# Optimization experiments

Measured on AMD Instinct MI355X. Metric: run time of the kernel, lower is better.

## Reference

```python
import jax, jax.numpy as jnp
import numpy as np

# Transformer config constants (from init_kwargs)
SRF = 3.0                 # spatial_receptive_field
SRF2 = SRF * SRF
ALPHA = 2.0
BETA = 8.0
GAMMA = 16.0
RES = jnp.array([0.5, 0.5, 0.5], dtype=jnp.float32)   # relative_positional_gresolution
N_BUCKETS = 2 * 8 + 1                                  # 2*beta + 1 = 17
MUL = jnp.array([N_BUCKETS ** 2, N_BUCKETS, 1], dtype=jnp.float32)  # [289,17,1]
SLICES_PER_ROT = 2


def setup_inputs() -> dict:
    key = jax.random.key(0)
    k1, k2 = jax.random.split(key)
    N = 3072
    # LiDAR-like point coordinates in a 10m cube; receptive field 3.0 makes radius filter selective
    xyz = jax.random.uniform(k1, (N, 3), dtype=jnp.float32) * 10.0
    # grid columns: [batch, block, gx, gy, gz]; values < 128 per the torch assert
    grid = jax.random.randint(k2, (N, 5), 0, 8, dtype=jnp.int32)
    return {"xyz": xyz, "grid": grid}


def _bucket_base(x):
    # from_dxyz_to_bucket_base, res.size(0)==3 branch
    x = x / RES
    x_abs = jnp.abs(x)
    log_ratio = jnp.log(jnp.maximum(x_abs, 1e-6) / ALPHA) / np.log(GAMMA / ALPHA)
    sup = jnp.minimum(jnp.round(ALPHA - (BETA - ALPHA) * log_ratio), BETA)
    sup = jnp.sign(x) * sup
    return BETA + jnp.where(x_abs <= ALPHA, jnp.round(x), sup)


def reference(xyz, grid):
    # no-kvp path of jit_compute_interactions, expressed as dense [N,N] pair masks
    batch = grid[:, 0]
    block = grid[:, 1]
    coords = grid[:, 2:]            # grid_look[:, 1:]

    # batch equality filter (meshgrid + batch==batch)
    batch_eq = batch[:, None] == batch[None, :]
    # causal block filter: block[iq] <= block[ik]
    block_le = block[:, None] <= block[None, :]

    # force_keep_neighbours: adjacent voxels within the same block
    coord_adj = jnp.max(jnp.abs(coords[:, None, :] - coords[None, :, :]), axis=-1) <= 1
    forcekeep = coord_adj & (block[:, None] == block[None, :])

    # coarse spatial hash on xy: ceil(xy / srf), neighbor cells only
    xy_coarse = jnp.ceil(xyz[:, :2] / SRF).astype(jnp.int32)
    keep_coarse = jnp.max(jnp.abs(xy_coarse[:, None, :] - xy_coarse[None, :, :]), axis=-1) <= 1

    # pairwise deltas (torch uses fp16 here; fp32 kept for numerical clarity) [N,N,3]
    dxyz = xyz[:, None, :] - xyz[None, :, :]
    keepr = jnp.sum(dxyz * dxyz, axis=-1) <= SRF2

    mask = batch_eq & block_le & (forcekeep | keep_coarse) & (forcekeep | keepr)

    dxyz_m = jnp.where(mask[..., None], dxyz, 0.0)

    # from_dxyz_to_bucket_mul: log-bucketize each axis, flatten via mul_buckets
    buckets = jnp.sum(MUL * _bucket_base(dxyz_m), axis=-1).astype(jnp.int32)
    buckets = jnp.where(mask, buckets, 0)

    # dscanid = scanid[ik] - scanid[iq], scanid = block // slices_per_rotation
    scanid = block // SLICES_PER_ROT
    dscanid = jnp.where(mask, scanid[None, :] - scanid[:, None], 0)

    return dxyz_m, buckets, dscanid, mask
```

## Files before the change

kernel.cpp:

```cpp
#include <hip/hip_runtime.h>
#include <cmath>


__device__ __forceinline__ float bucket_base(float v) {
    const float x  = v * 2.0f;
    const float xa = fabsf(x);
    if (xa <= 2.0f) {
        return 8.0f + rintf(x);
    }
    const float lr = logf(fmaxf(xa, 1e-6f) * 0.5f) / 2.0794415416798357f;
    const float sup = fminf(rintf(2.0f - 6.0f * lr), 8.0f);
    return 8.0f + ((x > 0.0f) ? sup : -sup);
}

__global__ __launch_bounds__(256) void pair_kernel(
    const float* __restrict__ xyz, const int* __restrict__ grid,
    float* __restrict__ out, int N) {
#pragma clang fp contract(off)
    const int jq = blockIdx.x * blockDim.x + threadIdx.x;
    const int j0 = jq << 2;
    const int i  = blockIdx.y;
    if (j0 >= N) return;

    const float xi = xyz[3 * i + 0];
    const float yi = xyz[3 * i + 1];
    const float zi = xyz[3 * i + 2];
    const int bat_i = grid[5 * i + 0];
    const int blk_i = grid[5 * i + 1];
    const int c0i = grid[5 * i + 2];
    const int c1i = grid[5 * i + 3];
    const int c2i = grid[5 * i + 4];
    const int xci = (int)ceilf(xi / 3.0f);
    const int yci = (int)ceilf(yi / 3.0f);
    const int scan_i = blk_i >> 1;

    const float4* pv = reinterpret_cast<const float4*>(xyz + (size_t)3 * j0);
    const float4 p0 = pv[0], p1 = pv[1], p2 = pv[2];
    const int4* gv = reinterpret_cast<const int4*>(grid + (size_t)5 * j0);
    const int4 g0 = gv[0], g1 = gv[1], g2 = gv[2], g3 = gv[3], g4 = gv[4];

    const float jx[4]  = {p0.x, p0.w, p1.z, p2.y};
    const float jy[4]  = {p0.y, p1.x, p1.w, p2.z};
    const float jz[4]  = {p0.z, p1.y, p2.x, p2.w};
    const int   jbat[4] = {g0.x, g1.y, g2.z, g3.w};
    const int   jblk[4] = {g0.y, g1.z, g2.w, g4.x};
    const int   jc0[4]  = {g0.z, g1.w, g3.x, g4.y};
    const int   jc1[4]  = {g0.w, g2.x, g3.y, g4.z};
    const int   jc2[4]  = {g1.x, g2.y, g3.z, g4.w};

    float dxm[4], dym[4], dzm[4];
    bool  mk[4];
    bool  any = false;
#pragma unroll
    for (int k = 0; k < 4; ++k) {
        const float dx = xi - jx[k];
        const float dy = yi - jy[k];
        const float dz = zi - jz[k];
        const bool batch_eq = (bat_i == jbat[k]);
        const bool block_le = (blk_i <= jblk[k]);
        const int  cadj = max(max(abs(c0i - jc0[k]), abs(c1i - jc1[k])),
                              abs(c2i - jc2[k]));
        const bool forcekeep = (cadj <= 1) && (blk_i == jblk[k]);
        const int xcj = (int)ceilf(jx[k] / 3.0f);
        const int ycj = (int)ceilf(jy[k] / 3.0f);
        const bool keep_coarse = max(abs(xci - xcj), abs(yci - ycj)) <= 1;
        const float d2 = dx * dx + dy * dy + dz * dz;
        const bool keepr = (d2 <= 9.0f);
        const bool m = batch_eq && block_le &&
                       (forcekeep || keep_coarse) && (forcekeep || keepr);
        mk[k] = m;
        any |= m;
        dxm[k] = m ? dx : 0.0f;
        dym[k] = m ? dy : 0.0f;
        dzm[k] = m ? dz : 0.0f;
    }

    const size_t NN   = (size_t)N * (size_t)N;
    const size_t base = (size_t)i * (size_t)N + (size_t)j0;
    float4* o_dxyz = reinterpret_cast<float4*>(out + 3 * base);
    float4* o_bkt  = reinterpret_cast<float4*>(out + NN * 3 + base);
    float4* o_dsc  = reinterpret_cast<float4*>(out + NN * 4 + base);
    float4* o_msk  = reinterpret_cast<float4*>(out + NN * 5 + base);

    if (__ballot(any ? 1 : 0) == 0ULL) {
        const float4 z = make_float4(0.0f, 0.0f, 0.0f, 0.0f);
        o_dxyz[0] = z; o_dxyz[1] = z; o_dxyz[2] = z;
        o_bkt[0]  = z; o_dsc[0]  = z; o_msk[0]  = z;
        return;
    }

    float bf[4], df[4], mf[4];
#pragma unroll
    for (int k = 0; k < 4; ++k) {
        if (mk[k]) {
            const float b0 = bucket_base(dxm[k]);
            const float b1 = bucket_base(dym[k]);
            const float b2 = bucket_base(dzm[k]);
            const float bsum = (289.0f * b0 + 17.0f * b1) + b2;
            bf[k] = (float)(int)bsum;
            df[k] = (float)((jblk[k] >> 1) - scan_i);
            mf[k] = 1.0f;
        } else {
            bf[k] = 0.0f; df[k] = 0.0f; mf[k] = 0.0f;
        }
    }

    o_dxyz[0] = make_float4(dxm[0], dym[0], dzm[0], dxm[1]);
    o_dxyz[1] = make_float4(dym[1], dzm[1], dxm[2], dym[2]);
    o_dxyz[2] = make_float4(dzm[2], dxm[3], dym[3], dzm[3]);
    o_bkt[0]  = make_float4(bf[0], bf[1], bf[2], bf[3]);
    o_dsc[0]  = make_float4(df[0], df[1], df[2], df[3]);
    o_msk[0]  = make_float4(mf[0], mf[1], mf[2], mf[3]);
}

extern "C" void kernel_launch(void* const* d_in, const int* in_sizes, int n_in,
                              void* d_out, int out_size, void* d_ws, size_t ws_size,
                              hipStream_t stream) {
    const float* xyz  = (const float*)d_in[0];
    const int*   grid = (const int*)d_in[1];
    float*       out  = (float*)d_out;
    const int N = in_sizes[0] / 3;

    const int BLOCK = 256;
    const int jquads = N / 4;
    dim3 gdim((jquads + BLOCK - 1) / BLOCK, N, 1);
    pair_kernel<<<gdim, dim3(BLOCK, 1, 1), 0, stream>>>(xyz, grid, out, N);
}
```

Baseline: 219.3 us.

## Stage j-point data in LDS and remap threads for coalesced stores

Each block now cooperatively loads a 1024-point chunk of xyz and grid into shared memory. Each thread then handles four j indices strided by 64 within its wavefront instead of four consecutive ones. The scalar outputs are written per element with the lanes of a wavefront coalesced, and the interleaved dxyz output is transposed through LDS so it can still be written as float4. This is meant to improve the store and load access pattern of this write-bound kernel, at the cost of extra LDS traffic, a barrier, and an implicit assumption that N is a multiple of 1024.

After: 215.9 us. Within noise of the previous version (-1.5%).

```diff
diff --git a/kernel.cpp b/kernel.cpp
--- a/kernel.cpp
+++ b/kernel.cpp
@@ -13,14 +13,31 @@
     return 8.0f + ((x > 0.0f) ? sup : -sup);
 }
 
+#define TPB 256
+#define JB  1024
+
 __global__ __launch_bounds__(256) void pair_kernel(
     const float* __restrict__ xyz, const int* __restrict__ grid,
     float* __restrict__ out, int N) {
 #pragma clang fp contract(off)
-    const int jq = blockIdx.x * blockDim.x + threadIdx.x;
-    const int j0 = jq << 2;
-    const int i  = blockIdx.y;
-    if (j0 >= N) return;
+    __shared__ float s_xyz[3 * JB];
+    __shared__ int   s_grid[5 * JB];
+    __shared__ float s_st[3 * JB];
+
+    const int tid = threadIdx.x;
+    const int i   = blockIdx.y;
+    const int J0  = blockIdx.x * JB;
+
+    {
+        const float4* gx = reinterpret_cast<const float4*>(xyz + (size_t)3 * J0);
+        float4* sx = reinterpret_cast<float4*>(s_xyz);
+#pragma unroll
+        for (int p = 0; p < 3; ++p) sx[TPB * p + tid] = gx[TPB * p + tid];
+        const int4* gg = reinterpret_cast<const int4*>(grid + (size_t)5 * J0);
+        int4* sg = reinterpret_cast<int4*>(s_grid);
+#pragma unroll
+        for (int p = 0; p < 5; ++p) sg[TPB * p + tid] = gg[TPB * p + tid];
+    }
 
     const float xi = xyz[3 * i + 0];
     const float yi = xyz[3 * i + 1];
@@ -34,35 +51,38 @@
     const int yci = (int)ceilf(yi / 3.0f);
     const int scan_i = blk_i >> 1;
 
-    const float4* pv = reinterpret_cast<const float4*>(xyz + (size_t)3 * j0);
-    const float4 p0 = pv[0], p1 = pv[1], p2 = pv[2];
-    const int4* gv = reinterpret_cast<const int4*>(grid + (size_t)5 * j0);
-    const int4 g0 = gv[0], g1 = gv[1], g2 = gv[2], g3 = gv[3], g4 = gv[4];
+    __syncthreads();
 
-    const float jx[4]  = {p0.x, p0.w, p1.z, p2.y};
-    const float jy[4]  = {p0.y, p1.x, p1.w, p2.z};
-    const float jz[4]  = {p0.z, p1.y, p2.x, p2.w};
-    const int   jbat[4] = {g0.x, g1.y, g2.z, g3.w};
-    const int   jblk[4] = {g0.y, g1.z, g2.w, g4.x};
-    const int   jc0[4]  = {g0.z, g1.w, g3.x, g4.y};
-    const int   jc1[4]  = {g0.w, g2.x, g3.y, g4.z};
-    const int   jc2[4]  = {g1.x, g2.y, g3.z, g4.w};
+    const int w   = tid >> 6;
+    const int l   = tid & 63;
+    const int jw0 = 256 * w;
 
     float dxm[4], dym[4], dzm[4];
+    int   jblkA[4];
     bool  mk[4];
     bool  any = false;
 #pragma unroll
     for (int k = 0; k < 4; ++k) {
-        const float dx = xi - jx[k];
-        const float dy = yi - jy[k];
-        const float dz = zi - jz[k];
-        const bool batch_eq = (bat_i == jbat[k]);
-        const bool block_le = (blk_i <= jblk[k]);
-        const int  cadj = max(max(abs(c0i - jc0[k]), abs(c1i - jc1[k])),
-                              abs(c2i - jc2[k]));
-        const bool forcekeep = (cadj <= 1) && (blk_i == jblk[k]);
-        const int xcj = (int)ceilf(jx[k] / 3.0f);
-        const int ycj = (int)ceilf(jy[k] / 3.0f);
+        const int jl = jw0 + 64 * k + l;
+        const float jx = s_xyz[3 * jl + 0];
+        const float jy = s_xyz[3 * jl + 1];
+        const float jz = s_xyz[3 * jl + 2];
+        const int jbat = s_grid[5 * jl + 0];
+        const int jblk = s_grid[5 * jl + 1];
+        const int jc0  = s_grid[5 * jl + 2];
+        const int jc1  = s_grid[5 * jl + 3];
+        const int jc2  = s_grid[5 * jl + 4];
+
+        const float dx = xi - jx;
+        const float dy = yi - jy;
+        const float dz = zi - jz;
+        const bool batch_eq = (bat_i == jbat);
+        const bool block_le = (blk_i <= jblk);
+        const int  cadj = max(max(abs(c0i - jc0), abs(c1i - jc1)),
+                              abs(c2i - jc2));
+        const bool forcekeep = (cadj <= 1) && (blk_i == jblk);
+        const int xcj = (int)ceilf(jx / 3.0f);
+        const int ycj = (int)ceilf(jy / 3.0f);
         const bool keep_coarse = max(abs(xci - xcj), abs(yci - ycj)) <= 1;
         const float d2 = dx * dx + dy * dy + dz * dz;
         const bool keepr = (d2 <= 9.0f);
@@ -70,47 +90,58 @@
                        (forcekeep || keep_coarse) && (forcekeep || keepr);
         mk[k] = m;
         any |= m;
+        jblkA[k] = jblk;
         dxm[k] = m ? dx : 0.0f;
         dym[k] = m ? dy : 0.0f;
         dzm[k] = m ? dz : 0.0f;
     }
 
-    const size_t NN   = (size_t)N * (size_t)N;
-    const size_t base = (size_t)i * (size_t)N + (size_t)j0;
-    float4* o_dxyz = reinterpret_cast<float4*>(out + 3 * base);
-    float4* o_bkt  = reinterpret_cast<float4*>(out + NN * 3 + base);
-    float4* o_dsc  = reinterpret_cast<float4*>(out + NN * 4 + base);
-    float4* o_msk  = reinterpret_cast<float4*>(out + NN * 5 + base);
+    const size_t NN      = (size_t)N * (size_t)N;
+    const size_t rowbase = (size_t)i * (size_t)N + (size_t)J0;
+    float* __restrict__ obkt = out + NN * 3 + rowbase;
+    float* __restrict__ odsc = out + NN * 4 + rowbase;
+    float* __restrict__ omsk = out + NN * 5 + rowbase;
+    float4* __restrict__ od4 =
+        reinterpret_cast<float4*>(out + 3 * (rowbase + (size_t)jw0));
 
     if (__ballot(any ? 1 : 0) == 0ULL) {
-        const float4 z = make_float4(0.0f, 0.0f, 0.0f, 0.0f);
-        o_dxyz[0] = z; o_dxyz[1] = z; o_dxyz[2] = z;
-        o_bkt[0]  = z; o_dsc[0]  = z; o_msk[0]  = z;
+        const float4 z4 = make_float4(0.0f, 0.0f, 0.0f, 0.0f);
+#pragma unroll
+        for (int p = 0; p < 3; ++p) od4[64 * p + l] = z4;
+#pragma unroll
+        for (int k = 0; k < 4; ++k) {
+            const int jl = jw0 + 64 * k + l;
+            obkt[jl] = 0.0f;
+            odsc[jl] = 0.0f;
+            omsk[jl] = 0.0f;
+        }
         return;
     }
 
-    float bf[4], df[4], mf[4];
 #pragma unroll
     for (int k = 0; k < 4; ++k) {
+        const int jl = jw0 + 64 * k + l;
+        float b = 0.0f, d = 0.0f, mvf = 0.0f;
         if (mk[k]) {
             const float b0 = bucket_base(dxm[k]);
             const float b1 = bucket_base(dym[k]);
             const float b2 = bucket_base(dzm[k]);
             const float bsum = (289.0f * b0 + 17.0f * b1) + b2;
-            bf[k] = (float)(int)bsum;
-            df[k] = (float)((jblk[k] >> 1) - scan_i);
-            mf[k] = 1.0f;
-        } else {
-            bf[k] = 0.0f; df[k] = 0.0f; mf[k] = 0.0f;
+            b   = (float)(int)bsum;
+            d   = (float)((jblkA[k] >> 1) - scan_i);
+            mvf = 1.0f;
         }
+        obkt[jl] = b;
+        odsc[jl] = d;
+        omsk[jl] = mvf;
+        s_st[3 * jl + 0] = dxm[k];
+        s_st[3 * jl + 1] = dym[k];
+        s_st[3 * jl + 2] = dzm[k];
     }
 
-    o_dxyz[0] = make_float4(dxm[0], dym[0], dzm[0], dxm[1]);
-    o_dxyz[1] = make_float4(dym[1], dzm[1], dxm[2], dym[2]);
-    o_dxyz[2] = make_float4(dzm[2], dxm[3], dym[3], dzm[3]);
-    o_bkt[0]  = make_float4(bf[0], bf[1], bf[2], bf[3]);
-    o_dsc[0]  = make_float4(df[0], df[1], df[2], df[3]);
-    o_msk[0]  = make_float4(mf[0], mf[1], mf[2], mf[3]);
+    const float4* st4 = reinterpret_cast<const float4*>(s_st + 3 * jw0);
+#pragma unroll
+    for (int p = 0; p < 3; ++p) od4[64 * p + l] = st4[64 * p + l];
 }
 
 extern "C" void kernel_launch(void* const* d_in, const int* in_sizes, int n_in,
@@ -121,8 +152,6 @@
     float*       out  = (float*)d_out;
     const int N = in_sizes[0] / 3;
 
-    const int BLOCK = 256;
-    const int jquads = N / 4;
-    dim3 gdim((jquads + BLOCK - 1) / BLOCK, N, 1);
-    pair_kernel<<<gdim, dim3(BLOCK, 1, 1), 0, stream>>>(xyz, grid, out, N);
+    dim3 gdim(N / JB, N, 1);
+    pair_kernel<<<gdim, dim3(TPB, 1, 1), 0, stream>>>(xyz, grid, out, N);
 }
```
